# Performance work log

Hardware: AMD Instinct MI355X
Metric: run time of the kernel (lower is better)

## Reference

```python
import jax, jax.numpy as jnp
import numpy as np

B, S, H = 4, 2048, 1024
EXP_BITS, SIG_BITS = 5, 10  # rmode=1 -> round-to-nearest


def quantize(x):
    """Simulated low-precision float quantization (LightChop-style) with STE.

    exp_bits exponent bits (bias = 2^(e-1)-1, exponent clamped -> subnormal
    handling falls out of the clamp), sig_bits significand bits, round-to-nearest.
    """
    bias = 2 ** (EXP_BITS - 1) - 1
    ax = jnp.abs(x)
    e = jnp.floor(jnp.log2(jnp.where(ax > 0, ax, 1.0)))
    e = jnp.clip(e, 1 - bias, bias)               # clamp to representable exponent range
    scale = jnp.exp2(e - SIG_BITS)                # ulp at this exponent
    q = jnp.round(x / scale) * scale              # round significand to SIG_BITS bits
    max_val = (2.0 - 2.0 ** (-SIG_BITS)) * 2.0 ** bias
    q = jnp.clip(q, -max_val, max_val)            # saturate overflow
    # straight-through estimator: forward = q, backward = identity
    return x + jax.lax.stop_gradient(q - x)


def setup_inputs() -> dict:
    key = jax.random.key(0)
    ks = jax.random.split(key, 7)
    w_scale = 1.0 / np.sqrt(H)
    return {
        "x": jax.random.normal(ks[0], (B, S, H), dtype=jnp.float32),
        "Wq": jax.random.normal(ks[1], (H, H), dtype=jnp.float32) * w_scale,
        "bq": jax.random.normal(ks[2], (H,), dtype=jnp.float32) * 0.01,
        "Wk": jax.random.normal(ks[3], (H, H), dtype=jnp.float32) * w_scale,
        "bk": jax.random.normal(ks[4], (H,), dtype=jnp.float32) * 0.01,
        "Wv": jax.random.normal(ks[5], (H, H), dtype=jnp.float32) * w_scale,
        "bv": jax.random.normal(ks[6], (H,), dtype=jnp.float32) * 0.01,
    }


def reference(x, Wq, bq, Wk, bk, Wv, bv):
    # nn.Linear: y = x @ W.T + b   (W stored [out, in])
    q = quantize(jnp.einsum("bsh,oh->bso", x, Wq) + bq)
    k = quantize(jnp.einsum("bsh,oh->bso", x, Wk) + bk)
    v = quantize(jnp.einsum("bsh,oh->bso", x, Wv) + bv)
    inv_sqrt_h = 1.0 / (H ** 0.5)
    scores = quantize(jnp.einsum("bsh,bth->bst", q, k) * inv_sqrt_h)  # [B,S,S]
    attn = quantize(jax.nn.softmax(scores, axis=-1))
    return jnp.einsum("bst,bth->bsh", attn, v)
```

## Files before the change

kernel.cpp:

```cpp
#include <hip/hip_runtime.h>
#include <hip/hip_fp16.h>

#define B_ 4
#define S_ 2048
#define H_ 1024
#define M_ (B_ * S_)

typedef _Float16 f16;
typedef _Float16 f16x8 __attribute__((ext_vector_type(8)));
typedef _Float16 f16x4 __attribute__((ext_vector_type(4)));
typedef float f32x4 __attribute__((ext_vector_type(4)));

typedef __attribute__((address_space(3))) unsigned int* lds_u32p;
typedef const __attribute__((address_space(1))) unsigned int* gbl_u32p;

__device__ __forceinline__ void stage16(const f16* g, f16* l) {
  __builtin_amdgcn_global_load_lds((gbl_u32p)g, (lds_u32p)l, 16, 0, 0);
}

__global__ __launch_bounds__(256) void downconvert_all(
    const float* __restrict__ x, const float* __restrict__ W0,
    const float* __restrict__ W1, const float* __restrict__ W2,
    f16* __restrict__ xh, f16* __restrict__ Wh) {
  const int b = blockIdx.x;
  const float* src;
  f16* dst;
  long i;
  if (b < M_ * H_ / 1024) {
    src = x; dst = xh;
    i = (long)b * 256 + threadIdx.x;
  } else {
    const int wb = b - M_ * H_ / 1024;
    const int sel = wb >> 10;
    src = sel == 0 ? W0 : (sel == 1 ? W1 : W2);
    dst = Wh + (long)sel * H_ * H_;
    i = (long)(wb & 1023) * 256 + threadIdx.x;
  }
  f32x4 v = ((const f32x4*)src)[i];
  f16x4 h;
#pragma unroll
  for (int c = 0; c < 4; c++) h[c] = (f16)v[c];
  ((f16x4*)dst)[i] = h;
}

__global__ __launch_bounds__(256, 2)
void qkv_gemm(const f16* __restrict__ xh, const f16* __restrict__ Wh,
              const float* __restrict__ bq, const float* __restrict__ bk,
              const float* __restrict__ bv, f16* __restrict__ qkv,
              f16* __restrict__ vT) {
  __shared__ __align__(16) f16 As[2 * 128 * 32];
  __shared__ __align__(16) f16 Bs[2 * 128 * 32];
  const int t = threadIdx.x;
  const int wave = t >> 6, lane = t & 63;
  const int quad = lane >> 4, l16 = lane & 15;
  const int wm = (wave & 1) * 64, wn = (wave >> 1) * 64;
  const int sel = blockIdx.y >> 3;
  const int ntile = (blockIdx.y & 7) * 128;
  const int mtile = blockIdx.x * 128;

  const f16* Ab = xh + (long)mtile * H_;
  const f16* Bb = Wh + (long)sel * H_ * H_ + (long)ntile * H_;

  const int r0 = t >> 2;
  const int c8 = (t & 3) * 8;

  f32x4 acc[4][4] = {};

  for (int k0 = 0; k0 < H_; k0 += 64) {
    __syncthreads();
    stage16(Ab + (long)r0 * H_ + k0 + c8,             As + t * 8);
    stage16(Ab + (long)(r0 + 64) * H_ + k0 + c8,      As + 2048 + t * 8);
    stage16(Ab + (long)r0 * H_ + k0 + 32 + c8,        As + 4096 + t * 8);
    stage16(Ab + (long)(r0 + 64) * H_ + k0 + 32 + c8, As + 6144 + t * 8);
    stage16(Bb + (long)r0 * H_ + k0 + c8,             Bs + t * 8);
    stage16(Bb + (long)(r0 + 64) * H_ + k0 + c8,      Bs + 2048 + t * 8);
    stage16(Bb + (long)r0 * H_ + k0 + 32 + c8,        Bs + 4096 + t * 8);
    stage16(Bb + (long)(r0 + 64) * H_ + k0 + 32 + c8, Bs + 6144 + t * 8);
    __syncthreads();
#pragma unroll
    for (int kk = 0; kk < 2; kk++) {
      f16x8 ah[4], bh[4];
#pragma unroll
      for (int i = 0; i < 4; i++) {
        ah[i] = *(const f16x8*)&As[kk * 4096 + (wm + i * 16 + l16) * 32 + quad * 8];
        bh[i] = *(const f16x8*)&Bs[kk * 4096 + (wn + i * 16 + l16) * 32 + quad * 8];
      }
#pragma unroll
      for (int i = 0; i < 4; i++)
#pragma unroll
        for (int j = 0; j < 4; j++)
          acc[i][j] = __builtin_amdgcn_mfma_f32_16x16x32_f16(ah[i], bh[j], acc[i][j], 0, 0, 0);
    }
  }

  const float* bias = sel == 0 ? bq : (sel == 1 ? bk : bv);
  if (sel == 2) {
#pragma unroll
    for (int j = 0; j < 4; j++) {
      int n = ntile + wn + j * 16 + l16;
      float bb = bias[n];
#pragma unroll
      for (int i = 0; i < 4; i++) {
        int m = mtile + wm + i * 16 + quad * 4;
        f16x4 pack;
#pragma unroll
        for (int r = 0; r < 4; r++) pack[r] = (f16)(acc[i][j][r] + bb);
        *(f16x4*)&vT[((long)(m >> 11) * H_ + n) * S_ + (m & 2047)] = pack;
      }
    }
  } else {
    f16* out = qkv + (long)sel * M_ * H_;
#pragma unroll
    for (int j = 0; j < 4; j++) {
      int n = ntile + wn + j * 16 + l16;
      float bb = bias[n];
#pragma unroll
      for (int i = 0; i < 4; i++) {
        int m = mtile + wm + i * 16 + quad * 4;
#pragma unroll
        for (int r = 0; r < 4; r++)
          out[(long)(m + r) * H_ + n] = (f16)(acc[i][j][r] + bb);
      }
    }
  }
}

template <int OUT_F16>
__global__ __launch_bounds__(256, 2)
void gemm_nt(const f16* __restrict__ A, const f16* __restrict__ Bm,
             void* __restrict__ C, int lda, int ldb, int ldc, int K,
             long sA, long sB, long sC, float alpha) {
  __shared__ __align__(16) f16 As[2 * 128 * 32];
  __shared__ __align__(16) f16 Bs[2 * 128 * 32];
  const int t = threadIdx.x;
  const int wave = t >> 6, lane = t & 63;
  const int quad = lane >> 4, l16 = lane & 15;
  const int wm = (wave & 1) * 64, wn = (wave >> 1) * 64;
  const f16* Ab = A + blockIdx.z * sA + (long)blockIdx.x * 128 * lda;
  const f16* Bb = Bm + blockIdx.z * sB + (long)blockIdx.y * 128 * ldb;
  const int r0 = t >> 2;
  const int c8 = ((t & 3) ^ ((r0 >> 1) & 3)) * 8;
  const int swz8 = (quad ^ ((l16 >> 1) & 3)) * 8;
  f32x4 acc[4][4] = {};
  for (int k0 = 0; k0 < K; k0 += 64) {
    __syncthreads();
    stage16(Ab + (long)r0 * lda + k0 + c8,             As + t * 8);
    stage16(Ab + (long)(r0 + 64) * lda + k0 + c8,      As + 2048 + t * 8);
    stage16(Ab + (long)r0 * lda + k0 + 32 + c8,        As + 4096 + t * 8);
    stage16(Ab + (long)(r0 + 64) * lda + k0 + 32 + c8, As + 6144 + t * 8);
    stage16(Bb + (long)r0 * ldb + k0 + c8,             Bs + t * 8);
    stage16(Bb + (long)(r0 + 64) * ldb + k0 + c8,      Bs + 2048 + t * 8);
    stage16(Bb + (long)r0 * ldb + k0 + 32 + c8,        Bs + 4096 + t * 8);
    stage16(Bb + (long)(r0 + 64) * ldb + k0 + 32 + c8, Bs + 6144 + t * 8);
    __syncthreads();
#pragma unroll
    for (int kk = 0; kk < 2; kk++) {
      f16x8 af[4], bf[4];
#pragma unroll
      for (int i = 0; i < 4; i++) {
        af[i] = *(const f16x8*)&As[kk * 4096 + (wm + i * 16 + l16) * 32 + swz8];
        bf[i] = *(const f16x8*)&Bs[kk * 4096 + (wn + i * 16 + l16) * 32 + swz8];
      }
#pragma unroll
      for (int i = 0; i < 4; i++)
#pragma unroll
        for (int j = 0; j < 4; j++)
          acc[i][j] = __builtin_amdgcn_mfma_f32_16x16x32_f16(af[i], bf[j], acc[i][j], 0, 0, 0);
    }
  }
  const long mb = (long)blockIdx.x * 128 + wm;
  const long nb = (long)blockIdx.y * 128 + wn;
#pragma unroll
  for (int i = 0; i < 4; i++)
#pragma unroll
    for (int j = 0; j < 4; j++) {
      long m = mb + i * 16 + quad * 4;
      long n = nb + j * 16 + l16;
#pragma unroll
      for (int r = 0; r < 4; r++) {
        float v = acc[i][j][r] * alpha;
        if (OUT_F16)
          ((f16*)C)[blockIdx.z * sC + (m + r) * ldc + n] = (f16)v;
        else
          ((float*)C)[blockIdx.z * sC + (m + r) * ldc + n] = v;
      }
    }
}

__global__ __launch_bounds__(256) void softmax_w(f16* __restrict__ sc) {
  const int wave = threadIdx.x >> 6, lane = threadIdx.x & 63;
  const long row = (long)blockIdx.x * 4 + wave;
  f16* p = sc + row * S_;
  f16x8 v[4];
#pragma unroll
  for (int i = 0; i < 4; ++i) v[i] = ((const f16x8*)p)[i * 64 + lane];
  float f[32];
  float m = -3.0e38f;
#pragma unroll
  for (int i = 0; i < 4; ++i)
#pragma unroll
    for (int c = 0; c < 8; ++c) {
      float x = (float)v[i][c];
      f[i * 8 + c] = x;
      m = fmaxf(m, x);
    }
#pragma unroll
  for (int o = 32; o > 0; o >>= 1) m = fmaxf(m, __shfl_xor(m, o));
  float s = 0.f;
#pragma unroll
  for (int i = 0; i < 32; ++i) { f[i] = __expf(f[i] - m); s += f[i]; }
#pragma unroll
  for (int o = 32; o > 0; o >>= 1) s += __shfl_xor(s, o);
  const float inv = 1.0f / s;
#pragma unroll
  for (int i = 0; i < 4; ++i) {
    f16x8 ov;
#pragma unroll
    for (int c = 0; c < 8; ++c) ov[c] = (f16)(f[i * 8 + c] * inv);
    ((f16x8*)p)[i * 64 + lane] = ov;
  }
}

extern "C" void kernel_launch(void* const* d_in, const int* in_sizes, int n_in,
                              void* d_out, int out_size, void* d_ws, size_t ws_size,
                              hipStream_t stream) {
  (void)in_sizes; (void)n_in; (void)out_size; (void)ws_size;
  const float* x  = (const float*)d_in[0];
  const float* Wq = (const float*)d_in[1];
  const float* bq = (const float*)d_in[2];
  const float* Wk = (const float*)d_in[3];
  const float* bk = (const float*)d_in[4];
  const float* Wv = (const float*)d_in[5];
  const float* bv = (const float*)d_in[6];

  char* ws = (char*)d_ws;
  f16* xh  = (f16*)ws; ws += (size_t)M_ * H_ * 2;
  f16* Wh  = (f16*)ws; ws += (size_t)3 * H_ * H_ * 2;
  f16* qkv = (f16*)ws; ws += (size_t)2 * M_ * H_ * 2;
  f16* vT  = (f16*)ws; ws += (size_t)B_ * H_ * S_ * 2;
  f16* sc  = (f16*)ws; ws += (size_t)B_ * S_ * S_ * 2;

  downconvert_all<<<M_ * H_ / 1024 + 3 * H_ * H_ / 1024, 256, 0, stream>>>(
      x, Wq, Wk, Wv, xh, Wh);

  qkv_gemm<<<dim3(64, 24), 256, 0, stream>>>(xh, Wh, bq, bk, bv, qkv, vT);

  gemm_nt<1><<<dim3(16, 16, 4), 256, 0, stream>>>(
      qkv, qkv + (size_t)M_ * H_, sc, H_, H_, S_, H_,
      (long)S_ * H_, (long)S_ * H_, (long)S_ * S_, 0.03125f);

  softmax_w<<<M_ / 4, 256, 0, stream>>>(sc);

  gemm_nt<0><<<dim3(16, 8, 4), 256, 0, stream>>>(
      sc, vT, d_out, S_, S_, H_, S_,
      (long)S_ * S_, (long)H_ * S_, (long)S_ * H_, 1.0f);
}
```

Baseline: 246.9 us.

## Fuse softmax into the PV GEMM with per-tile row statistics and on-the-fly exp

This drops the standalone softmax kernel. Each PV GEMM block now makes two passes over its 128 score rows to get the row max and log-sum-exp, stores them in shared memory, and then applies exp2 to the A fragments right before the MFMA calls. The aim is to skip the separate write and re-read of the normalized score matrix. In exchange, all 8 N-tile blocks of a row strip recompute the same row statistics, re-reading the scores many times. The exp work is also repeated on every A fragment inside the GEMM inner loop, and there is a leftover no-op loop that reads an uninitialized vector.

```diff
diff --git a/kernel.cpp b/kernel.cpp
--- a/kernel.cpp
+++ b/kernel.cpp
@@ -125,33 +125,31 @@
   }
 }
 
-template <int OUT_F16>
 __global__ __launch_bounds__(256, 2)
-void gemm_nt(const f16* __restrict__ A, const f16* __restrict__ Bm,
-             void* __restrict__ C, int lda, int ldb, int ldc, int K,
-             long sA, long sB, long sC, float alpha) {
+void score_gemm(const f16* __restrict__ A, const f16* __restrict__ Bm,
+                f16* __restrict__ C, float alpha) {
   __shared__ __align__(16) f16 As[2 * 128 * 32];
   __shared__ __align__(16) f16 Bs[2 * 128 * 32];
   const int t = threadIdx.x;
   const int wave = t >> 6, lane = t & 63;
   const int quad = lane >> 4, l16 = lane & 15;
   const int wm = (wave & 1) * 64, wn = (wave >> 1) * 64;
-  const f16* Ab = A + blockIdx.z * sA + (long)blockIdx.x * 128 * lda;
-  const f16* Bb = Bm + blockIdx.z * sB + (long)blockIdx.y * 128 * ldb;
+  const f16* Ab = A + (long)blockIdx.z * S_ * H_ + (long)blockIdx.x * 128 * H_;
+  const f16* Bb = Bm + (long)blockIdx.z * S_ * H_ + (long)blockIdx.y * 128 * H_;
   const int r0 = t >> 2;
   const int c8 = ((t & 3) ^ ((r0 >> 1) & 3)) * 8;
   const int swz8 = (quad ^ ((l16 >> 1) & 3)) * 8;
   f32x4 acc[4][4] = {};
-  for (int k0 = 0; k0 < K; k0 += 64) {
-    __syncthreads();
-    stage16(Ab + (long)r0 * lda + k0 + c8,             As + t * 8);
-    stage16(Ab + (long)(r0 + 64) * lda + k0 + c8,      As + 2048 + t * 8);
-    stage16(Ab + (long)r0 * lda + k0 + 32 + c8,        As + 4096 + t * 8);
-    stage16(Ab + (long)(r0 + 64) * lda + k0 + 32 + c8, As + 6144 + t * 8);
-    stage16(Bb + (long)r0 * ldb + k0 + c8,             Bs + t * 8);
-    stage16(Bb + (long)(r0 + 64) * ldb + k0 + c8,      Bs + 2048 + t * 8);
-    stage16(Bb + (long)r0 * ldb + k0 + 32 + c8,        Bs + 4096 + t * 8);
-    stage16(Bb + (long)(r0 + 64) * ldb + k0 + 32 + c8, Bs + 6144 + t * 8);
+  for (int k0 = 0; k0 < H_; k0 += 64) {
+    __syncthreads();
+    stage16(Ab + (long)r0 * H_ + k0 + c8,             As + t * 8);
+    stage16(Ab + (long)(r0 + 64) * H_ + k0 + c8,      As + 2048 + t * 8);
+    stage16(Ab + (long)r0 * H_ + k0 + 32 + c8,        As + 4096 + t * 8);
+    stage16(Ab + (long)(r0 + 64) * H_ + k0 + 32 + c8, As + 6144 + t * 8);
+    stage16(Bb + (long)r0 * H_ + k0 + c8,             Bs + t * 8);
+    stage16(Bb + (long)(r0 + 64) * H_ + k0 + c8,      Bs + 2048 + t * 8);
+    stage16(Bb + (long)r0 * H_ + k0 + 32 + c8,        Bs + 4096 + t * 8);
+    stage16(Bb + (long)(r0 + 64) * H_ + k0 + 32 + c8, Bs + 6144 + t * 8);
     __syncthreads();
 #pragma unroll
     for (int kk = 0; kk < 2; kk++) {
@@ -168,6 +166,7 @@
           acc[i][j] = __builtin_amdgcn_mfma_f32_16x16x32_f16(af[i], bf[j], acc[i][j], 0, 0, 0);
     }
   }
+  f16* Cz = C + (long)blockIdx.z * S_ * S_;
   const long mb = (long)blockIdx.x * 128 + wm;
   const long nb = (long)blockIdx.y * 128 + wn;
 #pragma unroll
@@ -177,48 +176,104 @@
       long m = mb + i * 16 + quad * 4;
       long n = nb + j * 16 + l16;
 #pragma unroll
-      for (int r = 0; r < 4; r++) {
-        float v = acc[i][j][r] * alpha;
-        if (OUT_F16)
-          ((f16*)C)[blockIdx.z * sC + (m + r) * ldc + n] = (f16)v;
-        else
-          ((float*)C)[blockIdx.z * sC + (m + r) * ldc + n] = v;
-      }
-    }
-}
-
-__global__ __launch_bounds__(256) void softmax_w(f16* __restrict__ sc) {
-  const int wave = threadIdx.x >> 6, lane = threadIdx.x & 63;
-  const long row = (long)blockIdx.x * 4 + wave;
-  f16* p = sc + row * S_;
-  f16x8 v[4];
-#pragma unroll
-  for (int i = 0; i < 4; ++i) v[i] = ((const f16x8*)p)[i * 64 + lane];
-  float f[32];
-  float m = -3.0e38f;
-#pragma unroll
-  for (int i = 0; i < 4; ++i)
-#pragma unroll
-    for (int c = 0; c < 8; ++c) {
-      float x = (float)v[i][c];
-      f[i * 8 + c] = x;
-      m = fmaxf(m, x);
-    }
-#pragma unroll
-  for (int o = 32; o > 0; o >>= 1) m = fmaxf(m, __shfl_xor(m, o));
-  float s = 0.f;
-#pragma unroll
-  for (int i = 0; i < 32; ++i) { f[i] = __expf(f[i] - m); s += f[i]; }
-#pragma unroll
-  for (int o = 32; o > 0; o >>= 1) s += __shfl_xor(s, o);
-  const float inv = 1.0f / s;
-#pragma unroll
-  for (int i = 0; i < 4; ++i) {
-    f16x8 ov;
-#pragma unroll
-    for (int c = 0; c < 8; ++c) ov[c] = (f16)(f[i * 8 + c] * inv);
-    ((f16x8*)p)[i * 64 + lane] = ov;
-  }
+      for (int r = 0; r < 4; r++)
+        Cz[(m + r) * S_ + n] = (f16)(acc[i][j][r] * alpha);
+    }
+}
+
+__global__ __launch_bounds__(256, 2)
+void pv_gemm(const f16* __restrict__ sc, const f16* __restrict__ vT,
+             float* __restrict__ out) {
+  __shared__ __align__(16) f16 As[2 * 128 * 32];
+  __shared__ __align__(16) f16 Bs[2 * 128 * 32];
+  __shared__ float rowc[128];
+  const int t = threadIdx.x;
+  const int wave = t >> 6, lane = t & 63;
+  const int quad = lane >> 4, l16 = lane & 15;
+  const int wm = (wave & 1) * 64, wn = (wave >> 1) * 64;
+  const int mtile = blockIdx.x * 128, ntile = blockIdx.y * 128;
+  const f16* Ab = sc + (long)blockIdx.z * S_ * S_ + (long)mtile * S_;
+  const f16* Bb = vT + (long)blockIdx.z * H_ * S_ + (long)ntile * S_;
+
+  {
+    const f16* rp = Ab + (long)(t >> 1) * S_ + (t & 1) * 1024;
+    float mx = -3.0e38f;
+#pragma unroll 4
+    for (int i = 0; i < 128; ++i) {
+      f16x8 v = ((const f16x8*)rp)[i];
+#pragma unroll
+      for (int c = 0; c < 8; ++c) mx = fmaxf(mx, (float)v[c]);
+    }
+    mx = fmaxf(mx, __shfl_xor(mx, 1));
+    float s = 0.f;
+#pragma unroll 4
+    for (int i = 0; i < 128; ++i) {
+      f16x8 v = ((const f16x8*)rp)[i];
+#pragma unroll
+      for (int c = 0; c < 8; ++c) s += __expf((float)v[c] - mx);
+    }
+    s += __shfl_xor(s, 1);
+    if ((t & 1) == 0) rowc[t >> 1] = -mx * 1.44269504f - __log2f(s);
+  }
+  __syncthreads();
+  float ca[4];
+#pragma unroll
+  for (int i = 0; i < 4; ++i) ca[i] = rowc[wm + i * 16 + l16];
+
+  const int r0 = t >> 2;
+  const int c8 = ((t & 3) ^ ((r0 >> 1) & 3)) * 8;
+  const int swz8 = (quad ^ ((l16 >> 1) & 3)) * 8;
+  f32x4 acc[4][4] = {};
+  for (int k0 = 0; k0 < S_; k0 += 64) {
+    __syncthreads();
+    stage16(Ab + (long)r0 * S_ + k0 + c8,             As + t * 8);
+    stage16(Ab + (long)(r0 + 64) * S_ + k0 + c8,      As + 2048 + t * 8);
+    stage16(Ab + (long)r0 * S_ + k0 + 32 + c8,        As + 4096 + t * 8);
+    stage16(Ab + (long)(r0 + 64) * S_ + k0 + 32 + c8, As + 6144 + t * 8);
+    stage16(Bb + (long)r0 * S_ + k0 + c8,             Bs + t * 8);
+    stage16(Bb + (long)(r0 + 64) * S_ + k0 + c8,      Bs + 2048 + t * 8);
+    stage16(Bb + (long)r0 * S_ + k0 + 32 + c8,        Bs + 4096 + t * 8);
+    stage16(Bb + (long)(r0 + 64) * S_ + k0 + 32 + c8, Bs + 6144 + t * 8);
+    __syncthreads();
+#pragma unroll
+    for (int kk = 0; kk < 2; kk++) {
+      f16x8 af[4], bf[4];
+#pragma unroll
+      for (int i = 0; i < 4; i++) {
+        af[i] = *(const f16x8*)&As[kk * 4096 + (wm + i * 16 + l16) * 32 + swz8];
+        bf[i] = *(const f16x8*)&Bs[kk * 4096 + (wn + i * 16 + l16) * 32 + swz8];
+      }
+#pragma unroll
+      for (int i = 0; i < 4; i++) {
+        f16x8 pf;
+#pragma unroll
+        for (int e = 0; e < 8; e++)
+          pf = (e == 0) ? pf : pf;
+#pragma unroll
+        for (int e = 0; e < 8; e++)
+          pf[e] = (f16)exp2f(fmaf((float)af[i][e], 1.44269504f, ca[i]));
+        af[i] = pf;
+      }
+#pragma unroll
+      for (int i = 0; i < 4; i++)
+#pragma unroll
+        for (int j = 0; j < 4; j++)
+          acc[i][j] = __builtin_amdgcn_mfma_f32_16x16x32_f16(af[i], bf[j], acc[i][j], 0, 0, 0);
+    }
+  }
+  float* Cz = out + (long)blockIdx.z * S_ * H_;
+  const long mb = (long)mtile + wm;
+  const long nb = (long)ntile + wn;
+#pragma unroll
+  for (int i = 0; i < 4; i++)
+#pragma unroll
+    for (int j = 0; j < 4; j++) {
+      long m = mb + i * 16 + quad * 4;
+      long n = nb + j * 16 + l16;
+#pragma unroll
+      for (int r = 0; r < 4; r++)
+        Cz[(m + r) * H_ + n] = acc[i][j][r];
+    }
 }
 
 extern "C" void kernel_launch(void* const* d_in, const int* in_sizes, int n_in,
@@ -245,13 +300,8 @@
 
   qkv_gemm<<<dim3(64, 24), 256, 0, stream>>>(xh, Wh, bq, bk, bv, qkv, vT);
 
-  gemm_nt<1><<<dim3(16, 16, 4), 256, 0, stream>>>(
-      qkv, qkv + (size_t)M_ * H_, sc, H_, H_, S_, H_,
-      (long)S_ * H_, (long)S_ * H_, (long)S_ * S_, 0.03125f);
-
-  softmax_w<<<M_ / 4, 256, 0, stream>>>(sc);
-
-  gemm_nt<0><<<dim3(16, 8, 4), 256, 0, stream>>>(
-      sc, vT, d_out, S_, S_, H_, S_,
-      (long)S_ * S_, (long)H_ * S_, (long)S_ * H_, 1.0f);
-}
+  score_gemm<<<dim3(16, 16, 4), 256, 0, stream>>>(
+      qkv, qkv + (size_t)M_ * H_, sc, 0.03125f);
+
+  pv_gemm<<<dim3(16, 8, 4), 256, 0, stream>>>(sc, vT, (float*)d_out);
+}
```

Measured after the change: 369.6 us. 49.7% more time.

## Fuse fp32-to-fp16 conversion into QKV GEMM staging, drop downconvert kernel

Applied to the files above, without the earlier changes.

Removes the separate downconvert kernel and its fp16 workspace buffers for x and the weights. The QKV GEMM now loads fp32 tiles into registers, converts them to fp16, and writes them to LDS, replacing the async global_load_lds path. This saves a launch and a full write and re-read of x and W in fp16. In exchange each GEMM tile reads twice as many bytes from global memory, and x is reconverted 24 times and each weight matrix 64 times. Loads now pass through registers with no overlap across the barrier.

```diff
diff --git a/kernel.cpp b/kernel.cpp
--- a/kernel.cpp
+++ b/kernel.cpp
@@ -18,33 +18,19 @@
   __builtin_amdgcn_global_load_lds((gbl_u32p)g, (lds_u32p)l, 16, 0, 0);
 }
 
-__global__ __launch_bounds__(256) void downconvert_all(
-    const float* __restrict__ x, const float* __restrict__ W0,
-    const float* __restrict__ W1, const float* __restrict__ W2,
-    f16* __restrict__ xh, f16* __restrict__ Wh) {
-  const int b = blockIdx.x;
-  const float* src;
-  f16* dst;
-  long i;
-  if (b < M_ * H_ / 1024) {
-    src = x; dst = xh;
-    i = (long)b * 256 + threadIdx.x;
-  } else {
-    const int wb = b - M_ * H_ / 1024;
-    const int sel = wb >> 10;
-    src = sel == 0 ? W0 : (sel == 1 ? W1 : W2);
-    dst = Wh + (long)sel * H_ * H_;
-    i = (long)(wb & 1023) * 256 + threadIdx.x;
-  }
-  f32x4 v = ((const f32x4*)src)[i];
-  f16x4 h;
-#pragma unroll
-  for (int c = 0; c < 4; c++) h[c] = (f16)v[c];
-  ((f16x4*)dst)[i] = h;
-}
+#define CVW(a, b, dst)                                                       \
+  {                                                                          \
+    f16x8 h_;                                                                \
+    h_[0] = (f16)(a)[0]; h_[1] = (f16)(a)[1];                                \
+    h_[2] = (f16)(a)[2]; h_[3] = (f16)(a)[3];                                \
+    h_[4] = (f16)(b)[0]; h_[5] = (f16)(b)[1];                                \
+    h_[6] = (f16)(b)[2]; h_[7] = (f16)(b)[3];                                \
+    *(f16x8*)(dst) = h_;                                                     \
+  }
 
 __global__ __launch_bounds__(256, 2)
-void qkv_gemm(const f16* __restrict__ xh, const f16* __restrict__ Wh,
+void qkv_gemm(const float* __restrict__ x, const float* __restrict__ Wq,
+              const float* __restrict__ Wk, const float* __restrict__ Wv,
               const float* __restrict__ bq, const float* __restrict__ bk,
               const float* __restrict__ bv, f16* __restrict__ qkv,
               f16* __restrict__ vT) {
@@ -58,8 +44,9 @@
   const int ntile = (blockIdx.y & 7) * 128;
   const int mtile = blockIdx.x * 128;
 
-  const f16* Ab = xh + (long)mtile * H_;
-  const f16* Bb = Wh + (long)sel * H_ * H_ + (long)ntile * H_;
+  const float* Wsel = sel == 0 ? Wq : (sel == 1 ? Wk : Wv);
+  const float* Ab = x + (long)mtile * H_;
+  const float* Bb = Wsel + (long)ntile * H_;
 
   const int r0 = t >> 2;
   const int c8 = (t & 3) * 8;
@@ -68,14 +55,27 @@
 
   for (int k0 = 0; k0 < H_; k0 += 64) {
     __syncthreads();
-    stage16(Ab + (long)r0 * H_ + k0 + c8,             As + t * 8);
-    stage16(Ab + (long)(r0 + 64) * H_ + k0 + c8,      As + 2048 + t * 8);
-    stage16(Ab + (long)r0 * H_ + k0 + 32 + c8,        As + 4096 + t * 8);
-    stage16(Ab + (long)(r0 + 64) * H_ + k0 + 32 + c8, As + 6144 + t * 8);
-    stage16(Bb + (long)r0 * H_ + k0 + c8,             Bs + t * 8);
-    stage16(Bb + (long)(r0 + 64) * H_ + k0 + c8,      Bs + 2048 + t * 8);
-    stage16(Bb + (long)r0 * H_ + k0 + 32 + c8,        Bs + 4096 + t * 8);
-    stage16(Bb + (long)(r0 + 64) * H_ + k0 + 32 + c8, Bs + 6144 + t * 8);
+    const float* pa0 = Ab + (long)r0 * H_ + k0 + c8;
+    const float* pa1 = Ab + (long)(r0 + 64) * H_ + k0 + c8;
+    const float* pb0 = Bb + (long)r0 * H_ + k0 + c8;
+    const float* pb1 = Bb + (long)(r0 + 64) * H_ + k0 + c8;
+    f32x4 r[16];
+    r[ 0] = ((const f32x4*)pa0)[0];        r[ 1] = ((const f32x4*)pa0)[1];
+    r[ 2] = ((const f32x4*)pa1)[0];        r[ 3] = ((const f32x4*)pa1)[1];
+    r[ 4] = ((const f32x4*)(pa0 + 32))[0]; r[ 5] = ((const f32x4*)(pa0 + 32))[1];
+    r[ 6] = ((const f32x4*)(pa1 + 32))[0]; r[ 7] = ((const f32x4*)(pa1 + 32))[1];
+    r[ 8] = ((const f32x4*)pb0)[0];        r[ 9] = ((const f32x4*)pb0)[1];
+    r[10] = ((const f32x4*)pb1)[0];        r[11] = ((const f32x4*)pb1)[1];
+    r[12] = ((const f32x4*)(pb0 + 32))[0]; r[13] = ((const f32x4*)(pb0 + 32))[1];
+    r[14] = ((const f32x4*)(pb1 + 32))[0]; r[15] = ((const f32x4*)(pb1 + 32))[1];
+    CVW(r[ 0], r[ 1], As + t * 8);
+    CVW(r[ 2], r[ 3], As + 2048 + t * 8);
+    CVW(r[ 4], r[ 5], As + 4096 + t * 8);
+    CVW(r[ 6], r[ 7], As + 6144 + t * 8);
+    CVW(r[ 8], r[ 9], Bs + t * 8);
+    CVW(r[10], r[11], Bs + 2048 + t * 8);
+    CVW(r[12], r[13], Bs + 4096 + t * 8);
+    CVW(r[14], r[15], Bs + 6144 + t * 8);
     __syncthreads();
 #pragma unroll
     for (int kk = 0; kk < 2; kk++) {
@@ -234,16 +234,12 @@
   const float* bv = (const float*)d_in[6];
 
   char* ws = (char*)d_ws;
-  f16* xh  = (f16*)ws; ws += (size_t)M_ * H_ * 2;
-  f16* Wh  = (f16*)ws; ws += (size_t)3 * H_ * H_ * 2;
   f16* qkv = (f16*)ws; ws += (size_t)2 * M_ * H_ * 2;
   f16* vT  = (f16*)ws; ws += (size_t)B_ * H_ * S_ * 2;
   f16* sc  = (f16*)ws; ws += (size_t)B_ * S_ * S_ * 2;
 
-  downconvert_all<<<M_ * H_ / 1024 + 3 * H_ * H_ / 1024, 256, 0, stream>>>(
-      x, Wq, Wk, Wv, xh, Wh);
-
-  qkv_gemm<<<dim3(64, 24), 256, 0, stream>>>(xh, Wh, bq, bk, bv, qkv, vT);
+  qkv_gemm<<<dim3(64, 24), 256, 0, stream>>>(
+      x, Wq, Wk, Wv, bq, bk, bv, qkv, vT);
 
   gemm_nt<1><<<dim3(16, 16, 4), 256, 0, stream>>>(
       qkv, qkv + (size_t)M_ * H_, sc, H_, H_, S_, H_,
```

New measurement: 270.7 us. 9.7% more time.
